# Kernel optimization log

Hardware: AMD Instinct MI355X
Metric: run time of the kernel (lower is better)

The kernel has to match this reference:

```python
import jax, jax.numpy as jnp
import numpy as np

K = 3
PAD = 1
STRIDE = 1
DIL = 1


def _bilinear_gather(feat, y, x):
    # feat: [B,C,H,W]; y,x: [B,KK,H,W] sampling coords -> [B,C,KK,H,W]
    B, C, H, W = feat.shape
    feat_flat = feat.reshape(B, C, H * W)
    y0 = jnp.floor(y)
    x0 = jnp.floor(x)
    out = jnp.zeros((B, C) + y.shape[1:], feat.dtype)
    for yi in (y0, y0 + 1.0):
        for xi in (x0, x0 + 1.0):
            wgt = (1.0 - jnp.abs(y - yi)) * (1.0 - jnp.abs(x - xi))
            valid = (yi >= 0) & (yi <= H - 1) & (xi >= 0) & (xi <= W - 1)
            yc = jnp.clip(yi, 0, H - 1).astype(jnp.int32)
            xc = jnp.clip(xi, 0, W - 1).astype(jnp.int32)
            idx = (yc * W + xc).reshape(B, 1, -1)  # [B,1,KK*H*W]
            g = jnp.take_along_axis(feat_flat, idx, axis=2).reshape(B, C, *y.shape[1:])
            out = out + g * (wgt * valid)[:, None]
    return out


def setup_inputs() -> dict:
    key = jax.random.key(0)
    k1, k2, k3, k4, k5 = jax.random.split(key, 5)
    B, Cin, Cout, H, W = 2, 256, 256, 96, 96
    x = jax.random.normal(k1, (B, Cin, H, W), jnp.float32)
    pw_w = jax.random.normal(k2, (Cout, Cin), jnp.float32) / np.sqrt(Cin)
    off_w = jax.random.normal(k3, (2 * K * K, Cout), jnp.float32) * 0.01
    off_b = jax.random.normal(k4, (2 * K * K,), jnp.float32) * 0.5
    dw_w = jax.random.normal(k5, (Cout, K, K), jnp.float32) / K
    return {"x": x, "pw_w": pw_w, "off_w": off_w, "off_b": off_b, "dw_w": dw_w}


def reference(x, pw_w, off_w, off_b, dw_w):
    B, _, H, W = x.shape
    C = pw_w.shape[0]
    # pointwise 1x1 conv (in_channels -> out_channels)
    xp = jnp.einsum("bchw,oc->bohw", x, pw_w)
    # offset 1x1 conv: [B, 2*K*K, H, W], layout (y,x) interleaved per kernel pos
    off = jnp.einsum("bchw,oc->bohw", xp, off_w) + off_b[None, :, None, None]
    off = off.reshape(B, K * K, 2, H, W)
    oy, ox = off[:, :, 0], off[:, :, 1]  # [B,KK,H,W]
    # base sampling grid per kernel position (stride 1, pad 1, dil 1)
    ky, kx = jnp.meshgrid(jnp.arange(K), jnp.arange(K), indexing="ij")
    ky = ky.reshape(-1).astype(jnp.float32)  # [KK]
    kx = kx.reshape(-1).astype(jnp.float32)
    gh = jnp.arange(H, dtype=jnp.float32) * STRIDE - PAD
    gw = jnp.arange(W, dtype=jnp.float32) * STRIDE - PAD
    base_y = gh[None, :, None] + (ky * DIL)[:, None, None]  # [KK,H,1]
    base_x = gw[None, None, :] + (kx * DIL)[:, None, None].transpose(0, 2, 1)  # [KK,1,W]
    y = base_y[None] + oy  # [B,KK,H,W]
    xc = base_x[None] + ox
    sampled = _bilinear_gather(xp, y, xc)  # [B,C,KK,H,W]
    out = jnp.einsum("bckhw,ck->bchw", sampled, dw_w.reshape(C, K * K))
    return out
```

## Files before the change

kernel.cpp:

```cpp
#include <hip/hip_runtime.h>
#include <hip/hip_bf16.h>

#define HWP 9216
#define HH  96
#define WW  96
#define CC  256
#define NB  2

typedef __attribute__((ext_vector_type(8))) short bf16x8;
typedef __attribute__((ext_vector_type(4))) float f32x4;

__device__ inline unsigned short f2bf(float f) {
  union { __hip_bfloat16 h; unsigned short u; } cvt;
  cvt.h = __float2bfloat16(f);
  return cvt.u;
}
__device__ inline float bf_lo(unsigned int u) { return __uint_as_float(u << 16); }
__device__ inline float bf_hi(unsigned int u) { return __uint_as_float(u & 0xffff0000u); }

__global__ __launch_bounds__(256) void k_prep(const float* __restrict__ pw,
                                              const float* __restrict__ ow,
                                              const float* __restrict__ dw,
                                              unsigned short* __restrict__ pwb,
                                              unsigned short* __restrict__ wb,
                                              float* __restrict__ dwt) {
  int i = (blockIdx.x * 256 + threadIdx.x) * 4;
  if (i < CC * CC) {
    float4 v = *(const float4*)(pw + i);
    ushort4 o = make_ushort4(f2bf(v.x), f2bf(v.y), f2bf(v.z), f2bf(v.w));
    *(ushort4*)(pwb + i) = o;
  } else if (i < CC * CC + 32 * 256) {
    int j = i - CC * CC;
    int row = j >> 8;
    ushort4 o = make_ushort4(0, 0, 0, 0);
    if (row < 18) {
      float4 v = *(const float4*)(ow + j);
      o = make_ushort4(f2bf(v.x), f2bf(v.y), f2bf(v.z), f2bf(v.w));
    }
    *(ushort4*)(wb + j) = o;
  } else {
    int j2 = i - (CC * CC + 32 * 256);
    if (j2 < 9 * 256) {
      int kk = j2 >> 8;
      int ch = j2 & 255;
      float4 v = make_float4(dw[(ch + 0) * 9 + kk], dw[(ch + 1) * 9 + kk],
                             dw[(ch + 2) * 9 + kk], dw[(ch + 3) * 9 + kk]);
      *(float4*)(dwt + j2) = v;
    }
  }
}

__global__ __launch_bounds__(256) void k_main(const float* __restrict__ x,
                                              const unsigned short* __restrict__ pwb,
                                              const unsigned short* __restrict__ wb,
                                              const float* __restrict__ off_b,
                                              unsigned short* __restrict__ xpb,
                                              float* __restrict__ offs) {
  __shared__ unsigned short As[32 * 40];
  __shared__ unsigned short Bs[256 * 40];
  __shared__ unsigned short Cs[32 * 264];

  int g   = blockIdx.x;
  int e   = g & 7;
  int idx = g >> 3;
  int b   = idx / 36;
  int m   = idx - b * 36;
  int pix0 = (e * 36 + m) * 32;

  int t    = threadIdx.x;
  int lane = t & 63;
  int w    = t >> 6;
  int mw = (w & 1) * 16;
  int nw = (w >> 1) * 128;
  int r = lane & 15, q = lane >> 4;

  f32x4 acc[8] = {};

  const float* xg = x + (size_t)b * CC * HWP + pix0;
  int sc = t >> 3;
  int sp = (t & 7) * 4;

  for (int k0 = 0; k0 < CC; k0 += 32) {
    f32x4 xv = __builtin_nontemporal_load((const f32x4*)(xg + (size_t)(k0 + sc) * HWP + sp));
    As[(sp + 0) * 40 + sc] = f2bf(xv.x);
    As[(sp + 1) * 40 + sc] = f2bf(xv.y);
    As[(sp + 2) * 40 + sc] = f2bf(xv.z);
    As[(sp + 3) * 40 + sc] = f2bf(xv.w);
    const unsigned short* bg = pwb + k0;
#pragma unroll
    for (int rep = 0; rep < 4; ++rep) {
      int n  = rep * 64 + (t >> 2);
      int c8 = (t & 3) * 8;
      *(uint4*)&Bs[n * 40 + c8] = *(const uint4*)(bg + n * 256 + c8);
    }
    __syncthreads();
    bf16x8 a = *(const bf16x8*)&As[(mw + r) * 40 + q * 8];
#pragma unroll
    for (int nt = 0; nt < 8; ++nt) {
      bf16x8 bb = *(const bf16x8*)&Bs[(nw + nt * 16 + r) * 40 + q * 8];
      acc[nt] = __builtin_amdgcn_mfma_f32_16x16x32_bf16(a, bb, acc[nt], 0, 0, 0);
    }
    __syncthreads();
  }

#pragma unroll
  for (int nt = 0; nt < 8; ++nt)
#pragma unroll
    for (int rr = 0; rr < 4; ++rr)
      Cs[(mw + q * 4 + rr) * 264 + nw + nt * 16 + r] = f2bf(acc[nt][rr]);
  __syncthreads();

  {
    int pix = t >> 3, c32 = (t & 7) * 32;
    unsigned short* o = xpb + ((size_t)b * HWP + pix0 + pix) * CC + c32;
#pragma unroll
    for (int j = 0; j < 4; ++j)
      *(uint4*)(o + j * 8) = *(const uint4*)&Cs[pix * 264 + c32 + j * 8];
  }

  {
    int mw2 = (w & 1) * 16;
    int nw2 = (w >> 1) * 16;
    f32x4 oacc = {};
#pragma unroll
    for (int ks = 0; ks < CC; ks += 32) {
      bf16x8 a = *(const bf16x8*)&Cs[(mw2 + r) * 264 + ks + q * 8];
      uint4 u = *(const uint4*)(wb + (nw2 + r) * 256 + ks + q * 8);
      bf16x8 bb;
      ((uint4*)&bb)[0] = u;
      oacc = __builtin_amdgcn_mfma_f32_16x16x32_bf16(a, bb, oacc, 0, 0, 0);
    }
    int o = nw2 + r;
    if (o < 18) {
      float ob = off_b[o];
      size_t base = ((size_t)b * HWP + pix0 + mw2 + q * 4) * 20 + o;
#pragma unroll
      for (int rr = 0; rr < 4; ++rr)
        offs[base + (size_t)rr * 20] = oacc[rr] + ob;
    }
  }
}

__global__ __launch_bounds__(256) void k_gather(const unsigned short* __restrict__ xp,
                                                const float* __restrict__ offs,
                                                const float* __restrict__ dwt,
                                                float* __restrict__ out) {
  __shared__ float Cs[16][257];
  __shared__ float4 Wt[16][9];
  __shared__ int4   Ad[16][9];

  int g   = blockIdx.x;
  int e   = g & 7;
  int idx = g >> 3;
  int b   = idx / 72;
  int m2  = idx - b * 72;
  int c   = e * 72 + m2;
  int pix0 = b * HWP + c * 16;

  int wave = threadIdx.x >> 6;
  int lane = threadIdx.x & 63;
  int c0 = lane * 4;

  int hw0 = pix0 - b * HWP;
  const unsigned short* xb = xp + (size_t)b * HWP * CC;
  const float* opb = offs + (size_t)pix0 * 20;

  {
    int tp = threadIdx.x;
    if (tp < 144) {
      int ip = tp / 9;
      int kk = tp - ip * 9;
      int hw = hw0 + ip;
      int h = hw / WW;
      int wq = hw - h * WW;
      float2 o2 = *(const float2*)(opb + ip * 20 + 2 * kk);
      float y = (float)(h + kk / 3 - 1) + o2.x;
      float x = (float)(wq + kk % 3 - 1) + o2.y;
      float y0f = floorf(y), x0f = floorf(x);
      float fy = y - y0f, fx = x - x0f;
      int y0 = (int)y0f, x0 = (int)x0f;
      int y1 = y0 + 1, x1 = x0 + 1;
      bool vy0 = (y0 >= 0) & (y0 < HH);
      bool vy1 = (y1 >= 0) & (y1 < HH);
      bool vx0 = (x0 >= 0) & (x0 < WW);
      bool vx1 = (x1 >= 0) & (x1 < WW);
      int y0c = y0 < 0 ? 0 : (y0 > HH - 1 ? HH - 1 : y0);
      int y1c = y1 < 0 ? 0 : (y1 > HH - 1 ? HH - 1 : y1);
      int x0c = x0 < 0 ? 0 : (x0 > WW - 1 ? WW - 1 : x0);
      int x1c = x1 < 0 ? 0 : (x1 > WW - 1 ? WW - 1 : x1);
      Wt[ip][kk] = make_float4(
          (1.f - fy) * (1.f - fx) * ((vy0 && vx0) ? 1.f : 0.f),
          (1.f - fy) * fx         * ((vy0 && vx1) ? 1.f : 0.f),
          fy * (1.f - fx)         * ((vy1 && vx0) ? 1.f : 0.f),
          fy * fx                 * ((vy1 && vx1) ? 1.f : 0.f));
      Ad[ip][kk] = make_int4((y0c * WW + x0c) * (CC * 2), (y0c * WW + x1c) * (CC * 2),
                             (y1c * WW + x0c) * (CC * 2), (y1c * WW + x1c) * (CC * 2));
    }
  }
  __syncthreads();

  const char* xbc = (const char*)xb;
  unsigned lb = (unsigned)(lane * 8);

  float acc[4][4] = {};
#pragma unroll
  for (int kk = 0; kk < 9; ++kk) {
    float4 dv = *(const float4*)(dwt + kk * 256 + c0);
#pragma unroll
    for (int p4 = 0; p4 < 4; ++p4) {
      int ip = wave * 4 + p4;
      float4 wv = Wt[ip][kk];
      int4 av = Ad[ip][kk];
      uint2 u00 = *(const uint2*)(xbc + ((unsigned)av.x + lb));
      uint2 u01 = *(const uint2*)(xbc + ((unsigned)av.y + lb));
      uint2 u10 = *(const uint2*)(xbc + ((unsigned)av.z + lb));
      uint2 u11 = *(const uint2*)(xbc + ((unsigned)av.w + lb));

      float s0 = wv.x * bf_lo(u00.x) + wv.y * bf_lo(u01.x) + wv.z * bf_lo(u10.x) + wv.w * bf_lo(u11.x);
      float s1 = wv.x * bf_hi(u00.x) + wv.y * bf_hi(u01.x) + wv.z * bf_hi(u10.x) + wv.w * bf_hi(u11.x);
      float s2 = wv.x * bf_lo(u00.y) + wv.y * bf_lo(u01.y) + wv.z * bf_lo(u10.y) + wv.w * bf_lo(u11.y);
      float s3 = wv.x * bf_hi(u00.y) + wv.y * bf_hi(u01.y) + wv.z * bf_hi(u10.y) + wv.w * bf_hi(u11.y);

      acc[p4][0] += dv.x * s0;
      acc[p4][1] += dv.y * s1;
      acc[p4][2] += dv.z * s2;
      acc[p4][3] += dv.w * s3;
    }
  }
#pragma unroll
  for (int p4 = 0; p4 < 4; ++p4)
    *(float4*)&Cs[wave * 4 + p4][c0] =
        make_float4(acc[p4][0], acc[p4][1], acc[p4][2], acc[p4][3]);
  __syncthreads();
  int ch = threadIdx.x;
  float* ob = out + (size_t)b * CC * HWP + (size_t)ch * HWP + hw0;
#pragma unroll
  for (int p4 = 0; p4 < 4; ++p4) {
    float4 v = make_float4(Cs[p4 * 4 + 0][ch], Cs[p4 * 4 + 1][ch],
                           Cs[p4 * 4 + 2][ch], Cs[p4 * 4 + 3][ch]);
    *(float4*)(ob + p4 * 4) = v;
  }
}

extern "C" void kernel_launch(void* const* d_in, const int* in_sizes, int n_in,
                              void* d_out, int out_size, void* d_ws, size_t ws_size,
                              hipStream_t stream) {
  (void)in_sizes; (void)n_in; (void)out_size; (void)ws_size;
  const float* x     = (const float*)d_in[0];
  const float* pw_w  = (const float*)d_in[1];
  const float* off_w = (const float*)d_in[2];
  const float* off_b = (const float*)d_in[3];
  const float* dw_w  = (const float*)d_in[4];
  float* out = (float*)d_out;

  char* ws = (char*)d_ws;
  unsigned short* xpb = (unsigned short*)ws;
  float* offs = (float*)(ws + 9437184);
  unsigned short* wb  = (unsigned short*)(ws + 10911744);
  unsigned short* pwb = (unsigned short*)(ws + 10928128);
  float* dwt          = (float*)(ws + 11059200);

  k_prep <<<75, 256, 0, stream>>>(pw_w, off_w, dw_w, pwb, wb, dwt);
  k_main <<<576, 256, 0, stream>>>(x, pwb, wb, off_b, xpb, offs);
  k_gather<<<1152, 256, 0, stream>>>(xpb, offs, dwt, out);
}
```

Baseline: 125.7 us.

## Double-buffer GEMM K-loop tiles in LDS with register prefetch

Converts the pointwise-conv GEMM main loop to a double-buffered scheme. The next K-tile of x and weights is loaded into registers before the MFMAs on the current tile run, then written to the alternate LDS buffer, so only one barrier per iteration remains. Cs is aliased onto Bs to keep the LDS footprint roughly unchanged. The cost is more registers held across the MFMA block, which may reduce occupancy.

```diff
diff --git a/kernel.cpp b/kernel.cpp
--- a/kernel.cpp
+++ b/kernel.cpp
@@ -56,9 +56,8 @@
                                               const float* __restrict__ off_b,
                                               unsigned short* __restrict__ xpb,
                                               float* __restrict__ offs) {
-  __shared__ unsigned short As[32 * 40];
-  __shared__ unsigned short Bs[256 * 40];
-  __shared__ unsigned short Cs[32 * 264];
+  __shared__ unsigned short As[2][32 * 40];
+  __shared__ unsigned short Bs[2][256 * 40];
 
   int g   = blockIdx.x;
   int e   = g & 7;
@@ -80,28 +79,59 @@
   int sc = t >> 3;
   int sp = (t & 7) * 4;
 
-  for (int k0 = 0; k0 < CC; k0 += 32) {
-    f32x4 xv = __builtin_nontemporal_load((const f32x4*)(xg + (size_t)(k0 + sc) * HWP + sp));
-    As[(sp + 0) * 40 + sc] = f2bf(xv.x);
-    As[(sp + 1) * 40 + sc] = f2bf(xv.y);
-    As[(sp + 2) * 40 + sc] = f2bf(xv.z);
-    As[(sp + 3) * 40 + sc] = f2bf(xv.w);
-    const unsigned short* bg = pwb + k0;
+  {
+    f32x4 xv = __builtin_nontemporal_load((const f32x4*)(xg + (size_t)sc * HWP + sp));
+    As[0][(sp + 0) * 40 + sc] = f2bf(xv.x);
+    As[0][(sp + 1) * 40 + sc] = f2bf(xv.y);
+    As[0][(sp + 2) * 40 + sc] = f2bf(xv.z);
+    As[0][(sp + 3) * 40 + sc] = f2bf(xv.w);
 #pragma unroll
     for (int rep = 0; rep < 4; ++rep) {
       int n  = rep * 64 + (t >> 2);
       int c8 = (t & 3) * 8;
-      *(uint4*)&Bs[n * 40 + c8] = *(const uint4*)(bg + n * 256 + c8);
+      *(uint4*)&Bs[0][n * 40 + c8] = *(const uint4*)(pwb + n * 256 + c8);
+    }
+  }
+  __syncthreads();
+
+  for (int kt = 0; kt < 8; ++kt) {
+    int cur = kt & 1;
+    f32x4 xv;
+    uint4 bu[4];
+    bool pre = (kt < 7);
+    if (pre) {
+      int k0 = (kt + 1) * 32;
+      xv = __builtin_nontemporal_load((const f32x4*)(xg + (size_t)(k0 + sc) * HWP + sp));
+#pragma unroll
+      for (int rep = 0; rep < 4; ++rep) {
+        int n  = rep * 64 + (t >> 2);
+        int c8 = (t & 3) * 8;
+        bu[rep] = *(const uint4*)(pwb + n * 256 + k0 + c8);
+      }
+    }
+    bf16x8 a = *(const bf16x8*)&As[cur][(mw + r) * 40 + q * 8];
+#pragma unroll
+    for (int nt = 0; nt < 8; ++nt) {
+      bf16x8 bb = *(const bf16x8*)&Bs[cur][(nw + nt * 16 + r) * 40 + q * 8];
+      acc[nt] = __builtin_amdgcn_mfma_f32_16x16x32_bf16(a, bb, acc[nt], 0, 0, 0);
+    }
+    if (pre) {
+      int nx = cur ^ 1;
+      As[nx][(sp + 0) * 40 + sc] = f2bf(xv.x);
+      As[nx][(sp + 1) * 40 + sc] = f2bf(xv.y);
+      As[nx][(sp + 2) * 40 + sc] = f2bf(xv.z);
+      As[nx][(sp + 3) * 40 + sc] = f2bf(xv.w);
+#pragma unroll
+      for (int rep = 0; rep < 4; ++rep) {
+        int n  = rep * 64 + (t >> 2);
+        int c8 = (t & 3) * 8;
+        *(uint4*)&Bs[nx][n * 40 + c8] = bu[rep];
+      }
     }
     __syncthreads();
-    bf16x8 a = *(const bf16x8*)&As[(mw + r) * 40 + q * 8];
-#pragma unroll
-    for (int nt = 0; nt < 8; ++nt) {
-      bf16x8 bb = *(const bf16x8*)&Bs[(nw + nt * 16 + r) * 40 + q * 8];
-      acc[nt] = __builtin_amdgcn_mfma_f32_16x16x32_bf16(a, bb, acc[nt], 0, 0, 0);
-    }
-    __syncthreads();
-  }
+  }
+
+  unsigned short* Cs = &Bs[0][0];
 
 #pragma unroll
   for (int nt = 0; nt < 8; ++nt)
```

Result: no change. 124.6 us (-0.8%).
